# Performance work log

Measured on AMD Instinct MI355X. Metric: run time of the kernel, lower is better.

The kernel has to match this reference:

```python
import jax, jax.numpy as jnp
import numpy as np

H = 768; NH = 12; DH = H // NH; E = 2; R = 128; B = 32; S = 512
SCALE = 1.0 / np.sqrt(DH)


def _mha_core(q, k, v, mask):
    # q,k,v: [B,S,H] projected; mask: [B,S] (1 = keep)
    b, s, _ = q.shape
    qh = q.reshape(b, s, NH, DH)
    kh = k.reshape(b, s, NH, DH)
    vh = v.reshape(b, s, NH, DH)
    scores = jnp.einsum('bqhd,bkhd->bhqk', qh, kh) * SCALE
    scores = scores + (1.0 - mask)[:, None, None, :] * (-10000.0)
    probs = jax.nn.softmax(scores, axis=-1)
    return jnp.einsum('bhqk,bkhd->bqhd', probs, vh).reshape(b, s, H)


def _forward(x, switch_w, switch_b, c_wq, c_bq, c_wk, c_bk, c_wv, c_bv, c_wo, c_bo,
             e_wq, e_bq, e_aq, e_gq, e_wk, e_bk, e_ak, e_gk, e_wv, e_bv, e_av, e_gv,
             e_wo, e_bo, attention_mask):
    # --- switch routing (per-sample, mean-pooled over sequence) ---
    logits = x.mean(axis=1) @ switch_w + switch_b          # [B,E]
    route_prob = jax.nn.softmax(logits, axis=-1)
    route_prob_max = route_prob.max(axis=-1)               # [B]
    routes = jnp.argmax(route_prob, axis=-1)               # [B]
    onehot = jax.nn.one_hot(routes, E, dtype=x.dtype)      # [B,E] dense equivalent of gather/scatter dispatch

    # --- LoRA attention experts (vmapped over experts) ---
    def lora_expert(wq, bq, aq, gq, wk, bk, ak, gk, wv, bv, av, gv, wo, bo):
        q = x @ wq + bq + (x @ aq) @ gq
        k = x @ wk + bk + (x @ ak) @ gk
        v = x @ wv + bv + (x @ av) @ gv
        return _mha_core(q, k, v, attention_mask) @ wo + bo   # [B,S,H]

    expert_out = jax.vmap(lora_expert)(e_wq, e_bq, e_aq, e_gq, e_wk, e_bk, e_ak, e_gk,
                                       e_wv, e_bv, e_av, e_gv, e_wo, e_bo)  # [E,B,S,H]
    routed = jnp.einsum('ebsh,be->bsh', expert_out, onehot)

    # scaling factor = p_max / stop_grad(p_max) (forward identity, grad path to router)
    scaling = (route_prob_max / jax.lax.stop_gradient(route_prob_max))[:, None, None]
    routed = routed * scaling

    # --- common (shared) attention expert ---
    q = x @ c_wq + c_bq
    k = x @ c_wk + c_bk
    v = x @ c_wv + c_bv
    common = _mha_core(q, k, v, attention_mask) @ c_wo + c_bo
    return routed + common


def setup_inputs() -> dict:
    key = jax.random.key(0)
    ks = jax.random.split(key, 32)
    std = 0.02
    def w(i, shape):
        return jax.random.normal(ks[i], shape, jnp.float32) * std
    z = lambda shape: jnp.zeros(shape, jnp.float32)
    return {
        'x': jax.random.normal(ks[0], (B, S, H), jnp.float32),
        'switch_w': w(1, (H, E)), 'switch_b': z((E,)),
        'c_wq': w(2, (H, H)), 'c_bq': z((H,)),
        'c_wk': w(3, (H, H)), 'c_bk': z((H,)),
        'c_wv': w(4, (H, H)), 'c_bv': z((H,)),
        'c_wo': w(5, (H, H)), 'c_bo': z((H,)),
        'e_wq': w(6, (E, H, H)), 'e_bq': z((E, H)),
        'e_aq': w(7, (E, H, R)), 'e_gq': w(8, (E, R, H)),
        'e_wk': w(9, (E, H, H)), 'e_bk': z((E, H)),
        'e_ak': w(10, (E, H, R)), 'e_gk': w(11, (E, R, H)),
        'e_wv': w(12, (E, H, H)), 'e_bv': z((E, H)),
        'e_av': w(13, (E, H, R)), 'e_gv': w(14, (E, R, H)),
        'e_wo': w(15, (E, H, H)), 'e_bo': z((E, H)),
        'attention_mask': jnp.ones((B, S), jnp.float32),
    }


def reference(x, switch_w, switch_b, c_wq, c_bq, c_wk, c_bk, c_wv, c_bv, c_wo, c_bo,
              e_wq, e_bq, e_aq, e_gq, e_wk, e_bk, e_ak, e_gk, e_wv, e_bv, e_av, e_gv,
              e_wo, e_bo, attention_mask):
    return _forward(x, switch_w, switch_b, c_wq, c_bq, c_wk, c_bk, c_wv, c_bv, c_wo, c_bo,
                    e_wq, e_bq, e_aq, e_gq, e_wk, e_bk, e_ak, e_gk, e_wv, e_bv, e_av, e_gv,
                    e_wo, e_bo, attention_mask)
```

## Files before the change

kernel.cpp:

```cpp
#include <hip/hip_runtime.h>
#include <hip/hip_bf16.h>

#define DEVINL __device__ __forceinline__

typedef __bf16 bf16x8 __attribute__((ext_vector_type(8)));
typedef float f32x4 __attribute__((ext_vector_type(4)));
typedef unsigned int u32x4 __attribute__((ext_vector_type(4)));
typedef unsigned short u16x8 __attribute__((ext_vector_type(8)));
typedef unsigned short u16x4 __attribute__((ext_vector_type(4)));

DEVINL unsigned short f2bf(float f) {
  __hip_bfloat16 h = __float2bfloat16(f);
  return __builtin_bit_cast(unsigned short, h);
}

DEVINL float bf2f(unsigned short u) {
  return __builtin_bit_cast(float, ((unsigned)u) << 16);
}

DEVINL f32x4 mfma16(bf16x8 a, bf16x8 b, f32x4 c) {
  return __builtin_amdgcn_mfma_f32_16x16x32_bf16(a, b, c, 0, 0, 0);
}

DEVINL void gload_lds16(const void* g, void* l) {
  __builtin_amdgcn_global_load_lds(
      (const __attribute__((address_space(1))) unsigned int*)g,
      (__attribute__((address_space(3))) unsigned int*)l, 16, 0, 0);
}

__global__ __launch_bounds__(256) void k_cvt(const float* __restrict__ x,
                                             u16x8* __restrict__ xb) {
  int i = blockIdx.x * 256 + threadIdx.x;
  const float* p = x + (size_t)i * 8;
  float4 a = *(const float4*)p;
  float4 b = *(const float4*)(p + 4);
  u16x8 o;
  o[0] = f2bf(a.x); o[1] = f2bf(a.y); o[2] = f2bf(a.z); o[3] = f2bf(a.w);
  o[4] = f2bf(b.x); o[5] = f2bf(b.y); o[6] = f2bf(b.z); o[7] = f2bf(b.w);
  xb[i] = o;
}

__global__ __launch_bounds__(256) void k_xsum(const float* __restrict__ x,
                                              float* __restrict__ xsum) {
  int b = blockIdx.x, sc = blockIdx.z;
  int h = blockIdx.y * 256 + threadIdx.x;
  float s = 0.f;
  const float* p = x + ((size_t)(b * 512 + sc * 128)) * 768 + h;
  for (int i = 0; i < 128; ++i) s += p[(size_t)i * 768];
  xsum[(sc * 32 + b) * 768 + h] = s;
}

__global__ __launch_bounds__(256) void k_route(const float* __restrict__ xsum,
                                               const float* __restrict__ sw,
                                               const float* __restrict__ sb,
                                               int* __restrict__ route) {
  int b = blockIdx.x, t = threadIdx.x;
  float l0 = 0.f, l1 = 0.f;
  for (int h = t; h < 768; h += 256) {
    float xm = (xsum[(0 * 32 + b) * 768 + h] + xsum[(1 * 32 + b) * 768 + h] +
                xsum[(2 * 32 + b) * 768 + h] + xsum[(3 * 32 + b) * 768 + h]) *
               (1.f / 512.f);
    l0 += xm * sw[h * 2 + 0];
    l1 += xm * sw[h * 2 + 1];
  }
#pragma unroll
  for (int off = 32; off; off >>= 1) {
    l0 += __shfl_down(l0, off);
    l1 += __shfl_down(l1, off);
  }
  __shared__ float s0[4], s1[4];
  int w = t >> 6;
  if ((t & 63) == 0) { s0[w] = l0; s1[w] = l1; }
  __syncthreads();
  if (t == 0) {
    float a0 = sb[0] + s0[0] + s0[1] + s0[2] + s0[3];
    float a1 = sb[1] + s1[0] + s1[1] + s1[2] + s1[3];
    route[b] = (a1 > a0) ? 1 : 0;
  }
}

__global__ __launch_bounds__(256) void k_wt(const float* __restrict__ cwq, const float* __restrict__ cwk,
                                            const float* __restrict__ cwv, const float* __restrict__ cwo,
                                            const float* __restrict__ ewo,
                                            const float* __restrict__ ewq, const float* __restrict__ ewk,
                                            const float* __restrict__ ewv,
                                            unsigned short* __restrict__ wtc,
                                            unsigned short* __restrict__ wtewo,
                                            unsigned short* __restrict__ wtexp) {
  __shared__ float t[32][33];
  int z = blockIdx.z;
  const float* src;
  unsigned short* dst;
  if (z < 4) {
    src = (z == 0) ? cwq : (z == 1) ? cwk : (z == 2) ? cwv : cwo;
    dst = wtc + (size_t)z * 589824;
  } else if (z < 6) {
    src = ewo + (size_t)(z - 4) * 589824;
    dst = wtewo + (size_t)(z - 4) * 589824;
  } else {
    int mat = (z - 6) >> 1, e = (z - 6) & 1;
    src = ((mat == 0) ? ewq : (mat == 1) ? ewk : ewv) + (size_t)e * 589824;
    dst = wtexp + (size_t)(mat * 2 + e) * 589824;
  }
  int k0 = blockIdx.x * 32, n0 = blockIdx.y * 32;
  int tid = threadIdx.x;
#pragma unroll
  for (int i = 0; i < 4; ++i) {
    int lin = tid + 256 * i; int kk = lin >> 5, nn = lin & 31;
    t[kk][nn] = src[(size_t)(k0 + kk) * 768 + n0 + nn];
  }
  __syncthreads();
#pragma unroll
  for (int i = 0; i < 4; ++i) {
    int lin = tid + 256 * i; int nn = lin >> 5, kk = lin & 31;
    dst[(size_t)(n0 + nn) * 768 + k0 + kk] = f2bf(t[kk][nn]);
  }
}

__global__ __launch_bounds__(256) void k_acvt(const float* __restrict__ eaq, const float* __restrict__ eak,
                                              const float* __restrict__ eav,
                                              unsigned short* __restrict__ abt) {
  int z = blockIdx.z;
  int mat = z >> 1, e = z & 1;
  const float* src = ((mat == 0) ? eaq : (mat == 1) ? eak : eav) + (size_t)e * 98304;
  unsigned short* dst = abt + (size_t)z * 98304;
  int i = blockIdx.x * 256 + threadIdx.x;
  const float* p = src + (size_t)i * 8;
  float4 a = *(const float4*)p;
  float4 b = *(const float4*)(p + 4);
  u16x8 o;
  o[0] = f2bf(a.x); o[1] = f2bf(a.y); o[2] = f2bf(a.z); o[3] = f2bf(a.w);
  o[4] = f2bf(b.x); o[5] = f2bf(b.y); o[6] = f2bf(b.z); o[7] = f2bf(b.w);
  *(u16x8*)(dst + (size_t)i * 8) = o;
}

__global__ __launch_bounds__(256) void k_gtr(const float* __restrict__ egq, const float* __restrict__ egk,
                                             const float* __restrict__ egv,
                                             unsigned short* __restrict__ gtb) {
  __shared__ float t[32][33];
  int z = blockIdx.z;
  int mat = z >> 1, e = z & 1;
  const float* src = ((mat == 0) ? egq : (mat == 1) ? egk : egv) + (size_t)e * 98304;
  unsigned short* dst = gtb + (size_t)z * 98304;
  int n0 = blockIdx.x * 32, r0 = blockIdx.y * 32;
  int tid = threadIdx.x;
#pragma unroll
  for (int i = 0; i < 4; ++i) {
    int lin = tid + 256 * i; int rr = lin >> 5, nn = lin & 31;
    t[rr][nn] = src[(size_t)(r0 + rr) * 768 + n0 + nn];
  }
  __syncthreads();
#pragma unroll
  for (int i = 0; i < 4; ++i) {
    int lin = tid + 256 * i; int nn = lin >> 5, rr = lin & 31;
    dst[(size_t)(n0 + nn) * 128 + r0 + rr] = f2bf(t[rr][nn]);
  }
}

__global__ __launch_bounds__(256) void k_mergemm(const unsigned short* __restrict__ gtb,
                                                 const unsigned short* __restrict__ abt,
                                                 const unsigned short* __restrict__ wtexp,
                                                 unsigned short* __restrict__ wte) {
  const int z = blockIdx.z;
  const int m0 = blockIdx.x * 128, n0 = blockIdx.y * 128;
  const unsigned short* Am = gtb + (size_t)z * 98304;
  const unsigned short* Bm = abt + (size_t)z * 98304;
  const unsigned short* Wt = wtexp + (size_t)z * 589824;
  unsigned short* dst = wte + (size_t)z * 589824;
  __shared__ __align__(16) unsigned short As[128 * 32];
  __shared__ __align__(16) unsigned short Bs[128 * 32];
  const int tid = threadIdx.x, w = tid >> 6, lane = tid & 63, g = lane >> 4, l15 = lane & 15;
  const int wr = (w >> 1) * 64, wc = (w & 1) * 64;
  f32x4 acc[4][4] = {};
  for (int k0 = 0; k0 < 128; k0 += 32) {
#pragma unroll
    for (int c = 0; c < 2; ++c) {
      int o = (w * 2 + c) * 1024 + lane * 16;
      int row = o >> 6, chunk = (o >> 4) & 3;
      gload_lds16(Am + (size_t)(m0 + row) * 128 + k0 + (chunk << 3),
                  (char*)As + (w * 2 + c) * 1024);
      gload_lds16(Bm + (size_t)(n0 + row) * 128 + k0 + (chunk << 3),
                  (char*)Bs + (w * 2 + c) * 1024);
    }
    __syncthreads();
    bf16x8 af[4], bfr[4];
#pragma unroll
    for (int mi = 0; mi < 4; ++mi) {
      int row = wr + mi * 16 + l15;
      af[mi] = *(const bf16x8*)((const char*)As + row * 64 + (g << 4));
    }
#pragma unroll
    for (int ni = 0; ni < 4; ++ni) {
      int row = wc + ni * 16 + l15;
      bfr[ni] = *(const bf16x8*)((const char*)Bs + row * 64 + (g << 4));
    }
#pragma unroll
    for (int mi = 0; mi < 4; ++mi)
#pragma unroll
      for (int ni = 0; ni < 4; ++ni)
        acc[mi][ni] = mfma16(af[mi], bfr[ni], acc[mi][ni]);
    __syncthreads();
  }
#pragma unroll
  for (int ni = 0; ni < 4; ++ni) {
    int col = n0 + wc + ni * 16 + l15;
#pragma unroll
    for (int mi = 0; mi < 4; ++mi) {
#pragma unroll
      for (int r = 0; r < 4; ++r) {
        int row = m0 + wr + mi * 16 + 4 * g + r;
        size_t idx = (size_t)row * 768 + col;
        dst[idx] = f2bf(acc[mi][ni][r] + bf2f(Wt[idx]));
      }
    }
  }
}

template <int MH, int KK, bool LOADB>
DEVINL void qphase(const unsigned short* As, const unsigned short* Bs,
                   bf16x8 (&bfr)[4], f32x4 (&acc)[8][4],
                   int wr, int wc, int g, int l15) {
  if (LOADB) {
#pragma unroll
    for (int nj = 0; nj < 4; ++nj) {
      int row = wc + nj * 16 + l15;
      bfr[nj] = *(const bf16x8*)((const char*)Bs + row * 128 + (((KK * 4 + g) ^ (row & 7)) << 4));
    }
  }
  bf16x8 af[4];
#pragma unroll
  for (int mi = 0; mi < 4; ++mi) {
    int row = wr + MH * 64 + mi * 16 + l15;
    af[mi] = *(const bf16x8*)((const char*)As + row * 128 + (((KK * 4 + g) ^ (row & 7)) << 4));
  }
  __builtin_amdgcn_s_setprio(1);
#pragma unroll
  for (int mi = 0; mi < 4; ++mi)
#pragma unroll
    for (int nj = 0; nj < 4; ++nj)
      acc[MH * 4 + mi][nj] = mfma16(af[mi], bfr[nj], acc[MH * 4 + mi][nj]);
  __builtin_amdgcn_s_setprio(0);
}

__global__ __launch_bounds__(512, 2) void k_gemm_qkv(
    const unsigned short* __restrict__ xb, const unsigned short* __restrict__ wtc,
    const unsigned short* __restrict__ wte,
    const float* __restrict__ cbq, const float* __restrict__ cbk, const float* __restrict__ cbv,
    const float* __restrict__ ebq, const float* __restrict__ ebk, const float* __restrict__ ebv,
    const int* __restrict__ route,
    unsigned short* __restrict__ qC, unsigned short* __restrict__ kC, unsigned short* __restrict__ vC,
    unsigned short* __restrict__ qE, unsigned short* __restrict__ kE, unsigned short* __restrict__ vE,
    int base_expert) {
  extern __shared__ __align__(16) unsigned short smem[];
  const int m0 = blockIdx.x * 256, n0 = blockIdx.y * 256;
  const int mat = blockIdx.z % 3;
  const int expert = base_expert + blockIdx.z / 3;
  const int b = m0 >> 9;
  const unsigned short* wt;
  const float* bias;
  if (!expert) {
    wt = wtc + (size_t)mat * 589824;
    bias = (mat == 0) ? cbq : (mat == 1) ? cbk : cbv;
  } else {
    int e = route[b];
    wt = wte + (size_t)(mat * 2 + e) * 589824;
    bias = ((mat == 0) ? ebq : (mat == 1) ? ebk : ebv) + e * 768;
  }
  unsigned short* outq = expert ? qE : qC;
  unsigned short* outk = expert ? kE : kC;
  unsigned short* vt   = expert ? vE : vC;
  const int tid = threadIdx.x, w = tid >> 6, lane = tid & 63, g = lane >> 4, l15 = lane & 15;
  const int wr = (w >> 2) * 128, wc = (w & 3) * 64;
  const int srow = lane >> 3, sslot = lane & 7;
  f32x4 acc[8][4] = {};

  auto stage_half = [&](int buf, int t, int h) {
    const unsigned short* src = (h < 2) ? xb : wt;
    int rowbase = (h < 2) ? (m0 + h * 128) : (n0 + (h - 2) * 128);
    unsigned short* lb = smem + buf * 32768 + ((h < 2) ? (h * 8192) : (16384 + (h - 2) * 8192));
    int k0 = t * 64;
#pragma unroll
    for (int c = 0; c < 2; ++c) {
      int rl = (w * 2 + c) * 8 + srow;
      int gc = (sslot ^ (rl & 7)) << 3;
      gload_lds16(src + (size_t)(rowbase + rl) * 768 + k0 + gc,
                  (char*)lb + (w * 2 + c) * 1024);
    }
  };

#pragma unroll
  for (int h = 0; h < 4; ++h) stage_half(0, 0, h);
  int cur = 0;
  for (int t = 0; t < 12; ++t) {
    const int nxt = cur ^ 1;
    const int tn = (t + 1 < 12) ? (t + 1) : 0;
    const unsigned short* As = smem + cur * 32768;
    const unsigned short* Bs = smem + cur * 32768 + 16384;
    bf16x8 bfr[4];
    stage_half(nxt, tn, 0);
    stage_half(nxt, tn, 2);
    asm volatile("s_waitcnt vmcnt(4)" ::: "memory");
    asm volatile("s_barrier" ::: "memory");
    qphase<0, 0, true>(As, Bs, bfr, acc, wr, wc, g, l15);
    stage_half(nxt, tn, 1);
    stage_half(nxt, tn, 3);
    asm volatile("s_barrier" ::: "memory");
    qphase<1, 0, false>(As, Bs, bfr, acc, wr, wc, g, l15);
    asm volatile("s_barrier" ::: "memory");
    qphase<0, 1, true>(As, Bs, bfr, acc, wr, wc, g, l15);
    asm volatile("s_barrier" ::: "memory");
    qphase<1, 1, false>(As, Bs, bfr, acc, wr, wc, g, l15);
    asm volatile("s_barrier" ::: "memory");
    cur = nxt;
  }
  __syncthreads();

  if (mat != 2) {
    unsigned short* pw = smem + w * 8192;
#pragma unroll
    for (int nj = 0; nj < 4; ++nj) {
      float bv = bias[n0 + wc + nj * 16 + l15];
#pragma unroll
      for (int fr = 0; fr < 8; ++fr)
#pragma unroll
        for (int r = 0; r < 4; ++r) {
          int lr = fr * 16 + 4 * g + r;
          int lc = nj * 16 + l15;
          pw[lr * 64 + (((lc >> 3) ^ (lr & 7)) << 3) + (lc & 7)] =
              f2bf(acc[fr][nj][r] + bv);
        }
    }
    unsigned short* dst = (mat == 0) ? outq : outk;
#pragma unroll
    for (int i = 0; i < 16; ++i) {
      int ci = i * 64 + lane;
      int row = ci >> 3;
      int c8 = ci & 7;
      u16x8 v = *(const u16x8*)(pw + row * 64 + ((c8 ^ (row & 7)) << 3));
      *(u16x8*)(dst + (size_t)(m0 + wr + row) * 768 + n0 + wc + c8 * 8) = v;
    }
  } else {
    unsigned short* Ts2 = smem;
#pragma unroll
    for (int p = 0; p < 2; ++p) {
      if (((w & 3) >> 1) == p) {
#pragma unroll
        for (int nj = 0; nj < 4; ++nj) {
          int ccl = ((w & 3) & 1) * 64 + nj * 16 + l15;
          float bv = bias[n0 + p * 128 + ccl];
#pragma unroll
          for (int fr = 0; fr < 8; ++fr)
#pragma unroll
            for (int r = 0; r < 4; ++r) {
              int row = wr + fr * 16 + 4 * g + r;
              Ts2[ccl * 264 + row] = f2bf(acc[fr][nj][r] + bv);
            }
        }
      }
      __syncthreads();
#pragma unroll
      for (int i = 0; i < 8; ++i) {
        int ci = tid + 512 * i, cc = ci >> 5, j = ci & 31;
        u16x8 v = *(const u16x8*)(Ts2 + cc * 264 + j * 8);
        int colg = n0 + p * 128 + cc;
        int head = colg >> 6, dh = colg & 63;
        *(u16x8*)(vt + ((size_t)((b * 12 + head) * 64 + dh)) * 512 + (m0 & 511) + j * 8) = v;
      }
      __syncthreads();
    }
  }
}

__global__ __launch_bounds__(512) void k_attn(
    const unsigned short* __restrict__ Q0, const unsigned short* __restrict__ K0,
    const unsigned short* __restrict__ V0, unsigned short* __restrict__ ctx0,
    const unsigned short* __restrict__ Q1, const unsigned short* __restrict__ K1,
    const unsigned short* __restrict__ V1, unsigned short* __restrict__ ctx1,
    const float* __restrict__ mask) {
  const int qh = blockIdx.x, h = blockIdx.y;
  const int b = blockIdx.z & 31, path = blockIdx.z >> 5;
  const unsigned short* Q = path ? Q1 : Q0;
  const unsigned short* K = path ? K1 : K0;
  const unsigned short* Vt = path ? V1 : V0;
  unsigned short* ctx = path ? ctx1 : ctx0;
  const int tid = threadIdx.x, w = tid >> 6, lane = tid & 63, g = lane >> 4, l15 = lane & 15;
  const int qbase = b * 512 + qh * 256 + w * 32;
  bf16x8 qf[2][2];
#pragma unroll
  for (int qs = 0; qs < 2; ++qs) {
    const unsigned short* qp = Q + (size_t)(qbase + qs * 16 + l15) * 768 + h * 64;
    qf[qs][0] = *(const bf16x8*)(qp + g * 8);
    qf[qs][1] = *(const bf16x8*)(qp + 32 + g * 8);
  }
  __shared__ __align__(16) unsigned short Ks[64 * 64];
  __shared__ __align__(16) unsigned short Vs[64 * 64];
  __shared__ float mk2[512];
  float lsum[2] = {0.f, 0.f};
  f32x4 acc[2][4] = {};
  const unsigned short* Kb = K + (size_t)(b * 512) * 768 + h * 64;
  const unsigned short* Vb = Vt + (size_t)((b * 12 + h) * 64) * 512;
  const int srow = w * 8 + (lane >> 3);
  const int schunk = lane & 7;
  const int ssw = (schunk ^ (srow & 7)) << 3;
  const float C = 0.125f * 1.44269504f;
  mk2[tid] = (1.f - mask[b * 512 + tid]) * (-14426.9504f);
  for (int kt = 0; kt < 8; ++kt) {
    const int kv0 = kt * 64;
    gload_lds16(Kb + (size_t)(kv0 + srow) * 768 + ssw, (char*)Ks + w * 1024);
    gload_lds16(Vb + (size_t)srow * 512 + kv0 + ssw, (char*)Vs + w * 1024);
    __syncthreads();
#pragma unroll
    for (int qs = 0; qs < 2; ++qs) {
      f32x4 sf[4];
#pragma unroll
      for (int mb = 0; mb < 4; ++mb) {
        int row = mb * 16 + l15;
        bf16x8 ka  = *(const bf16x8*)(Ks + row * 64 + ((g ^ (row & 7)) << 3));
        bf16x8 kb2 = *(const bf16x8*)(Ks + row * 64 + (((g + 4) ^ (row & 7)) << 3));
        f32x4 z = {0.f, 0.f, 0.f, 0.f};
        z = mfma16(ka, qf[qs][0], z);
        z = mfma16(kb2, qf[qs][1], z);
        sf[mb] = z;
      }
      float p[16];
      float psum = 0.f;
#pragma unroll
      for (int mb = 0; mb < 4; ++mb)
#pragma unroll
        for (int r = 0; r < 4; ++r) {
          float e2 = exp2f(fmaf(sf[mb][r], C, mk2[kv0 + mb * 16 + g * 4 + r]));
          p[mb * 4 + r] = e2;
          psum += e2;
        }
      lsum[qs] += psum;
      unsigned pk[4][2];
#pragma unroll
      for (int mb = 0; mb < 4; ++mb)
#pragma unroll
        for (int hh = 0; hh < 2; ++hh)
          pk[mb][hh] = (unsigned)f2bf(p[mb * 4 + 2 * hh]) |
                       ((unsigned)f2bf(p[mb * 4 + 2 * hh + 1]) << 16);
#pragma unroll
      for (int ks = 0; ks < 2; ++ks) {
        unsigned pb[4];
#pragma unroll
        for (int j = 0; j < 4; ++j) {
          int src = l15 + 16 * ((2 * g + (j >> 1)) & 3);
          unsigned t0 = __shfl(pk[2 * ks + 0][j & 1], src);
          unsigned t1 = __shfl(pk[2 * ks + 1][j & 1], src);
          pb[j] = (g >> 1) ? t1 : t0;
        }
        u32x4 pbv = {pb[0], pb[1], pb[2], pb[3]};
        bf16x8 pf = __builtin_bit_cast(bf16x8, pbv);
#pragma unroll
        for (int d = 0; d < 4; ++d) {
          int row = d * 16 + l15;
          bf16x8 vf = *(const bf16x8*)(Vs + row * 64 + (((g + 4 * ks) ^ (row & 7)) << 3));
          acc[qs][d] = mfma16(vf, pf, acc[qs][d]);
        }
      }
    }
    __syncthreads();
  }
#pragma unroll
  for (int qs = 0; qs < 2; ++qs) {
    float t = lsum[qs];
    t += __shfl_xor(t, 16);
    t += __shfl_xor(t, 32);
    float inv = 1.f / t;
    unsigned short* op = ctx + (size_t)(qbase + qs * 16 + l15) * 768 + h * 64;
#pragma unroll
    for (int d = 0; d < 4; ++d) {
      u16x4 o4;
#pragma unroll
      for (int r = 0; r < 4; ++r) o4[r] = f2bf(acc[qs][d][r] * inv);
      *(u16x4*)(op + d * 16 + 4 * g) = o4;
    }
  }
}

__global__ __launch_bounds__(512, 2) void k_gemm_out(
    const unsigned short* __restrict__ ctxc, const unsigned short* __restrict__ ctxe,
    const unsigned short* __restrict__ woc, const unsigned short* __restrict__ woe,
    const float* __restrict__ cbo, const float* __restrict__ ebo,
    const int* __restrict__ route, float* __restrict__ out) {
  extern __shared__ __align__(16) unsigned short smem[];
  const int m0 = blockIdx.x * 256, n0 = blockIdx.y * 256;
  const int b = m0 >> 9;
  const int e = route[b];
  const int tid = threadIdx.x, w = tid >> 6, lane = tid & 63, g = lane >> 4, l15 = lane & 15;
  const int wr = (w >> 2) * 128, wc = (w & 3) * 64;
  const int srow = lane >> 3, sslot = lane & 7;
  f32x4 acc[8][4] = {};

  auto stage_half = [&](int buf, int t, int h) {
    const unsigned short* src =
        (h < 2) ? ((t < 12) ? ctxc : ctxe)
                : ((t < 12) ? woc : (woe + (size_t)e * 589824));
    int rowbase = (h < 2) ? (m0 + h * 128) : (n0 + (h - 2) * 128);
    unsigned short* lb = smem + buf * 32768 + ((h < 2) ? (h * 8192) : (16384 + (h - 2) * 8192));
    int k0 = (t % 12) * 64;
#pragma unroll
    for (int c = 0; c < 2; ++c) {
      int rl = (w * 2 + c) * 8 + srow;
      int gc = (sslot ^ (rl & 7)) << 3;
      gload_lds16(src + (size_t)(rowbase + rl) * 768 + k0 + gc,
                  (char*)lb + (w * 2 + c) * 1024);
    }
  };

#pragma unroll
  for (int h = 0; h < 4; ++h) stage_half(0, 0, h);
  int cur = 0;
  for (int t = 0; t < 24; ++t) {
    const int nxt = cur ^ 1;
    const int tn = (t + 1 < 24) ? (t + 1) : 0;
    const unsigned short* As = smem + cur * 32768;
    const unsigned short* Bs = smem + cur * 32768 + 16384;
    bf16x8 bfr[4];
    stage_half(nxt, tn, 0);
    stage_half(nxt, tn, 2);
    asm volatile("s_waitcnt vmcnt(4)" ::: "memory");
    asm volatile("s_barrier" ::: "memory");
    qphase<0, 0, true>(As, Bs, bfr, acc, wr, wc, g, l15);
    stage_half(nxt, tn, 1);
    stage_half(nxt, tn, 3);
    asm volatile("s_barrier" ::: "memory");
    qphase<1, 0, false>(As, Bs, bfr, acc, wr, wc, g, l15);
    asm volatile("s_barrier" ::: "memory");
    qphase<0, 1, true>(As, Bs, bfr, acc, wr, wc, g, l15);
    asm volatile("s_barrier" ::: "memory");
    qphase<1, 1, false>(As, Bs, bfr, acc, wr, wc, g, l15);
    asm volatile("s_barrier" ::: "memory");
    cur = nxt;
  }
  __syncthreads();

  float* fs = (float*)smem;
#pragma unroll
  for (int p = 0; p < 4; ++p) {
    if ((w >> 2) == (p >> 1)) {
#pragma unroll
      for (int nj = 0; nj < 4; ++nj) {
        int lc = wc + nj * 16 + l15;
        int col = n0 + lc;
        float bsum = cbo[col] + ebo[e * 768 + col];
#pragma unroll
        for (int fi = 0; fi < 4; ++fi) {
          int fr = (p & 1) * 4 + fi;
#pragma unroll
          for (int r = 0; r < 4; ++r) {
            int lr = fi * 16 + 4 * g + r;
            fs[lr * 256 + (((lc >> 2) ^ (lr & 7)) << 2) + (lc & 3)] =
                acc[fr][nj][r] + bsum;
          }
        }
      }
    }
    __syncthreads();
#pragma unroll
    for (int j = 0; j < 8; ++j) {
      int ci = j * 512 + tid;
      int row = ci >> 6, sl = ci & 63;
      f32x4 v = *(const f32x4*)(fs + row * 256 + ((sl ^ (row & 7)) << 2));
      *(f32x4*)(out + (size_t)(m0 + p * 64 + row) * 768 + n0 + sl * 4) = v;
    }
    __syncthreads();
  }
}

extern "C" void kernel_launch(void* const* d_in, const int* in_sizes, int n_in,
                              void* d_out, int out_size, void* d_ws, size_t ws_size,
                              hipStream_t stream) {
  const float* x    = (const float*)d_in[0];
  const float* sw   = (const float*)d_in[1];
  const float* sb   = (const float*)d_in[2];
  const float* cwq  = (const float*)d_in[3];
  const float* cbq  = (const float*)d_in[4];
  const float* cwk  = (const float*)d_in[5];
  const float* cbk  = (const float*)d_in[6];
  const float* cwv  = (const float*)d_in[7];
  const float* cbv  = (const float*)d_in[8];
  const float* cwo  = (const float*)d_in[9];
  const float* cbo  = (const float*)d_in[10];
  const float* ewq  = (const float*)d_in[11];
  const float* ebq  = (const float*)d_in[12];
  const float* eaq  = (const float*)d_in[13];
  const float* egq  = (const float*)d_in[14];
  const float* ewk  = (const float*)d_in[15];
  const float* ebk  = (const float*)d_in[16];
  const float* eak  = (const float*)d_in[17];
  const float* egk  = (const float*)d_in[18];
  const float* ewv  = (const float*)d_in[19];
  const float* ebv  = (const float*)d_in[20];
  const float* eav  = (const float*)d_in[21];
  const float* egv  = (const float*)d_in[22];
  const float* ewo  = (const float*)d_in[23];
  const float* ebo  = (const float*)d_in[24];
  const float* amask = (const float*)d_in[25];
  (void)in_sizes; (void)n_in; (void)out_size;

  (void)hipFuncSetAttribute(reinterpret_cast<const void*>(k_gemm_qkv),
                            hipFuncAttributeMaxDynamicSharedMemorySize, 131072);
  (void)hipFuncSetAttribute(reinterpret_cast<const void*>(k_gemm_out),
                            hipFuncAttributeMaxDynamicSharedMemorySize, 131072);

  char* ws = (char*)d_ws;
  const size_t SZ = 25165824;
  const size_t MERGED_NEED = 8 * SZ + 4718592 + 7077888 + 2359296 + 393216 + 256;
  const bool merged = (ws_size >= MERGED_NEED);

  unsigned short *xb, *qbC, *kC, *vC, *qbE, *kE, *vE, *ctxc, *ctxe;
  char* wbase;
  if (merged) {
    xb   = (unsigned short*)(ws);
    qbC  = (unsigned short*)(ws + SZ);
    kC   = (unsigned short*)(ws + 2 * SZ);
    vC   = (unsigned short*)(ws + 3 * SZ);
    qbE  = (unsigned short*)(ws + 4 * SZ);
    kE   = (unsigned short*)(ws + 5 * SZ);
    vE   = (unsigned short*)(ws + 6 * SZ);
    ctxc = (unsigned short*)(ws + 7 * SZ);
    ctxe = (unsigned short*)(ws);
    wbase = ws + 8 * SZ;
  } else {
    xb   = (unsigned short*)(ws);
    qbC  = qbE = (unsigned short*)(ws + SZ);
    kC   = kE  = (unsigned short*)(ws + 2 * SZ);
    vC   = vE  = (unsigned short*)(ws + 3 * SZ);
    ctxc = (unsigned short*)(ws + 4 * SZ);
    ctxe = (unsigned short*)(ws);
    wbase = ws + 5 * SZ;
  }
  unsigned short* wtc   = (unsigned short*)(wbase);
  unsigned short* wte   = (unsigned short*)(wbase + 4718592);
  unsigned short* wtewo = (unsigned short*)(wbase + 4718592 + 7077888);
  float* xsum           = (float*)(wbase + 4718592 + 7077888 + 2359296);
  int* route            = (int*)(wbase + 4718592 + 7077888 + 2359296 + 393216);
  unsigned short* abt   = (unsigned short*)(ws + SZ);
  unsigned short* gtb   = (unsigned short*)(ws + SZ + 1179648);
  unsigned short* wtexp = (unsigned short*)(ws + SZ + 2359296);

  k_cvt<<<6144, 256, 0, stream>>>(x, (u16x8*)xb);
  k_xsum<<<dim3(32, 3, 4), 256, 0, stream>>>(x, xsum);
  k_route<<<32, 256, 0, stream>>>(xsum, sw, sb, route);
  k_wt<<<dim3(24, 24, 12), 256, 0, stream>>>(cwq, cwk, cwv, cwo, ewo, ewq, ewk, ewv,
                                             wtc, wtewo, wtexp);
  k_acvt<<<dim3(48, 1, 6), 256, 0, stream>>>(eaq, eak, eav, abt);
  k_gtr<<<dim3(24, 4, 6), 256, 0, stream>>>(egq, egk, egv, gtb);
  k_mergemm<<<dim3(6, 6, 6), 256, 0, stream>>>(gtb, abt, wtexp, wte);

  if (merged) {
    k_gemm_qkv<<<dim3(64, 3, 6), 512, 131072, stream>>>(
        xb, wtc, wte, cbq, cbk, cbv, ebq, ebk, ebv, route,
        qbC, kC, vC, qbE, kE, vE, 0);
    k_attn<<<dim3(2, 12, 64), 512, 0, stream>>>(qbC, kC, vC, ctxc,
                                                qbE, kE, vE, ctxe, amask);
  } else {
    k_gemm_qkv<<<dim3(64, 3, 3), 512, 131072, stream>>>(
        xb, wtc, wte, cbq, cbk, cbv, ebq, ebk, ebv, route,
        qbC, kC, vC, qbC, kC, vC, 0);
    k_attn<<<dim3(2, 12, 32), 512, 0, stream>>>(qbC, kC, vC, ctxc,
                                                qbC, kC, vC, ctxc, amask);
    k_gemm_qkv<<<dim3(64, 3, 3), 512, 131072, stream>>>(
        xb, wtc, wte, cbq, cbk, cbv, ebq, ebk, ebv, route,
        qbC, kC, vC, qbC, kC, vC, 1);
    k_attn<<<dim3(2, 12, 32), 512, 0, stream>>>(qbC, kC, vC, ctxe,
                                                qbC, kC, vC, ctxe, amask);
  }
  k_gemm_out<<<dim3(64, 3), 512, 131072, stream>>>(ctxc, ctxe, wtc + 3 * 589824, wtewo,
                                                   cbo, ebo, route, (float*)d_out);
}
```

Baseline: 322.3 us.

## Fuse bf16 convert with sequence sum and cut GEMM mainloop barriers

Merges the fp32-to-bf16 conversion of x with the per-chunk sequence sum into one kernel, so x is read once and one launch is dropped. The fused kernel writes 2-byte bf16 values column-strided, which may coalesce less well than the old vectorized conversion. In both GEMM mainloops, all four next-tile stage loads are now issued up front with a looser vmcnt wait, and the intermediate barriers between the four compute phases are removed, keeping one barrier at each end of the iteration. This reduces synchronisation stalls and lets loads overlap the whole compute phase, at the cost of a single wait point per tile.

```diff
diff --git a/kernel.cpp b/kernel.cpp
--- a/kernel.cpp
+++ b/kernel.cpp
@@ -28,25 +28,21 @@
       (__attribute__((address_space(3))) unsigned int*)l, 16, 0, 0);
 }
 
-__global__ __launch_bounds__(256) void k_cvt(const float* __restrict__ x,
-                                             u16x8* __restrict__ xb) {
-  int i = blockIdx.x * 256 + threadIdx.x;
-  const float* p = x + (size_t)i * 8;
-  float4 a = *(const float4*)p;
-  float4 b = *(const float4*)(p + 4);
-  u16x8 o;
-  o[0] = f2bf(a.x); o[1] = f2bf(a.y); o[2] = f2bf(a.z); o[3] = f2bf(a.w);
-  o[4] = f2bf(b.x); o[5] = f2bf(b.y); o[6] = f2bf(b.z); o[7] = f2bf(b.w);
-  xb[i] = o;
-}
-
-__global__ __launch_bounds__(256) void k_xsum(const float* __restrict__ x,
-                                              float* __restrict__ xsum) {
+__global__ __launch_bounds__(256) void k_cvtsum(const float* __restrict__ x,
+                                                unsigned short* __restrict__ xb,
+                                                float* __restrict__ xsum) {
   int b = blockIdx.x, sc = blockIdx.z;
   int h = blockIdx.y * 256 + threadIdx.x;
+  size_t base = ((size_t)(b * 512 + sc * 128)) * 768 + h;
+  const float* p = x + base;
+  unsigned short* q = xb + base;
   float s = 0.f;
-  const float* p = x + ((size_t)(b * 512 + sc * 128)) * 768 + h;
-  for (int i = 0; i < 128; ++i) s += p[(size_t)i * 768];
+#pragma unroll 4
+  for (int i = 0; i < 128; ++i) {
+    float v = p[(size_t)i * 768];
+    s += v;
+    q[(size_t)i * 768] = f2bf(v);
+  }
   xsum[(sc * 32 + b) * 768 + h] = s;
 }
 
@@ -297,18 +293,13 @@
     const unsigned short* As = smem + cur * 32768;
     const unsigned short* Bs = smem + cur * 32768 + 16384;
     bf16x8 bfr[4];
-    stage_half(nxt, tn, 0);
-    stage_half(nxt, tn, 2);
-    asm volatile("s_waitcnt vmcnt(4)" ::: "memory");
+#pragma unroll
+    for (int h = 0; h < 4; ++h) stage_half(nxt, tn, h);
+    asm volatile("s_waitcnt vmcnt(8)" ::: "memory");
     asm volatile("s_barrier" ::: "memory");
-    qphase<0, 0, true>(As, Bs, bfr, acc, wr, wc, g, l15);
-    stage_half(nxt, tn, 1);
-    stage_half(nxt, tn, 3);
-    asm volatile("s_barrier" ::: "memory");
+    qphase<0, 0, true >(As, Bs, bfr, acc, wr, wc, g, l15);
     qphase<1, 0, false>(As, Bs, bfr, acc, wr, wc, g, l15);
-    asm volatile("s_barrier" ::: "memory");
-    qphase<0, 1, true>(As, Bs, bfr, acc, wr, wc, g, l15);
-    asm volatile("s_barrier" ::: "memory");
+    qphase<0, 1, true >(As, Bs, bfr, acc, wr, wc, g, l15);
     qphase<1, 1, false>(As, Bs, bfr, acc, wr, wc, g, l15);
     asm volatile("s_barrier" ::: "memory");
     cur = nxt;
@@ -518,18 +509,13 @@
     const unsigned short* As = smem + cur * 32768;
     const unsigned short* Bs = smem + cur * 32768 + 16384;
     bf16x8 bfr[4];
-    stage_half(nxt, tn, 0);
-    stage_half(nxt, tn, 2);
-    asm volatile("s_waitcnt vmcnt(4)" ::: "memory");
+#pragma unroll
+    for (int h = 0; h < 4; ++h) stage_half(nxt, tn, h);
+    asm volatile("s_waitcnt vmcnt(8)" ::: "memory");
     asm volatile("s_barrier" ::: "memory");
-    qphase<0, 0, true>(As, Bs, bfr, acc, wr, wc, g, l15);
-    stage_half(nxt, tn, 1);
-    stage_half(nxt, tn, 3);
-    asm volatile("s_barrier" ::: "memory");
+    qphase<0, 0, true >(As, Bs, bfr, acc, wr, wc, g, l15);
     qphase<1, 0, false>(As, Bs, bfr, acc, wr, wc, g, l15);
-    asm volatile("s_barrier" ::: "memory");
-    qphase<0, 1, true>(As, Bs, bfr, acc, wr, wc, g, l15);
-    asm volatile("s_barrier" ::: "memory");
+    qphase<0, 1, true >(As, Bs, bfr, acc, wr, wc, g, l15);
     qphase<1, 1, false>(As, Bs, bfr, acc, wr, wc, g, l15);
     asm volatile("s_barrier" ::: "memory");
     cur = nxt;
@@ -641,8 +627,7 @@
   unsigned short* gtb   = (unsigned short*)(ws + SZ + 1179648);
   unsigned short* wtexp = (unsigned short*)(ws + SZ + 2359296);
 
-  k_cvt<<<6144, 256, 0, stream>>>(x, (u16x8*)xb);
-  k_xsum<<<dim3(32, 3, 4), 256, 0, stream>>>(x, xsum);
+  k_cvtsum<<<dim3(32, 3, 4), 256, 0, stream>>>(x, xb, xsum);
   k_route<<<32, 256, 0, stream>>>(xsum, sw, sb, route);
   k_wt<<<dim3(24, 24, 12), 256, 0, stream>>>(cwq, cwk, cwv, cwo, ewo, ewq, ewk, ewv,
                                              wtc, wtewo, wtexp);
```

New measurement: 343.0 us. +6.4%, slower.
